# Performance work log

Hardware: AMD Instinct MI355X
Metric: run time of the kernel (lower is better)

## Reference

```python
import jax, jax.numpy as jnp
import numpy as np

B, D, H = 8192, 1024, 1024


def _linear_init(key, shape, fan_in):
    bound = 1.0 / np.sqrt(fan_in)
    return jax.random.uniform(key, shape, jnp.float32, -bound, bound)


def setup_inputs() -> dict:
    key = jax.random.key(0)
    ks = jax.random.split(key, 20)
    inp = {
        "x": jax.random.normal(ks[0], (B, D), jnp.float32),
        "h_prev": jax.random.normal(ks[1], (B, H), jnp.float32),
        "c_prev": jax.random.normal(ks[2], (B, H), jnp.float32),
        "C_prev": jax.random.normal(ks[3], (B, H), jnp.float32),
        "n_prev": jax.random.uniform(ks[4], (B, H), jnp.float32),
        "m_prev": jax.random.normal(ks[5], (B, H), jnp.float32),
    }
    # input projections Wz/Wi/Wf/Wo: Linear(D -> H) with bias
    for i, g in enumerate("ziofo"[:4]):
        pass
    names = ["z", "i", "f", "o"]
    for j, g in enumerate(names):
        inp[f"W{g}"] = _linear_init(ks[6 + j], (H, D), D)
        inp[f"b{g}"] = _linear_init(ks[10 + j], (H,), D)
        inp[f"R{g}"] = _linear_init(ks[14 + j], (H, H), H)  # no bias
    return inp


def reference(x, h_prev, c_prev, C_prev, n_prev, m_prev,
              Wz, bz, Wi, bi, Wf, bf, Wo, bo,
              Rz, Ri, Rf, Ro):
    # Batch the 4 input projections and 4 recurrent projections into 2 GEMMs.
    Wcat = jnp.concatenate([Wi, Wf, Wo, Wz], axis=0)        # [4H, D]
    bcat = jnp.concatenate([bi, bf, bo, bz], axis=0)        # [4H]
    Rcat = jnp.concatenate([Ri, Rf, Ro, Rz], axis=0)        # [4H, H]
    pre = x @ Wcat.T + bcat + h_prev @ Rcat.T               # [B, 4H]
    pi, pf, po, pz = jnp.split(pre, 4, axis=1)

    i = jnp.exp(pi)
    f = jax.nn.sigmoid(pf)
    o = jax.nn.sigmoid(po)
    z = jnp.tanh(pz)

    c = f * c_prev + i * z
    n = f * n_prev + i
    m = jnp.maximum(jnp.log(f) + m_prev, pi)  # log(exp(pi)) == pi
    h = o * (c / n)
    return (h, c, C_prev, n, m)
```

## Files before the change

kernel.cpp:

```cpp
#include <hip/hip_runtime.h>


#define B_SZ 8192
#define D_SZ 1024
#define H_SZ 1024
#define K_SZ 2048
#define N4H  4096

typedef __attribute__((ext_vector_type(4))) float f32x4;
typedef _Float16 f16;
typedef __attribute__((ext_vector_type(8))) f16 f16x8;
typedef unsigned short u16;
typedef __attribute__((ext_vector_type(4))) unsigned short u16x4;

static __device__ __forceinline__ u16 f2h(float f) {
    f16 h = (f16)f;
    return __builtin_bit_cast(unsigned short, h);
}

static __device__ __forceinline__ void load_lds16(const void* g, void* l) {
    __builtin_amdgcn_global_load_lds(
        (const __attribute__((address_space(1))) void*)g,
        (__attribute__((address_space(3))) void*)l, 16, 0, 0);
}

__global__ void convert_A(const float* __restrict__ x, const float* __restrict__ h,
                          u16* __restrict__ A) {
    const size_t nvec = (size_t)B_SZ * K_SZ / 4;
    const size_t stride = (size_t)gridDim.x * blockDim.x;
    for (size_t v = (size_t)blockIdx.x * blockDim.x + threadIdx.x; v < nvec; v += stride) {
        size_t e = v * 4;
        size_t row = e >> 11;
        int col = (int)(e & 2047);
        const float* src = (col < D_SZ) ? (x + row * D_SZ + col)
                                        : (h + row * H_SZ + (col - D_SZ));
        f32x4 val = *(const f32x4*)src;
        u16x4 o;
        o[0] = f2h(val[0]); o[1] = f2h(val[1]); o[2] = f2h(val[2]); o[3] = f2h(val[3]);
        *(u16x4*)(A + e) = o;
    }
}

__global__ void convert_W(const float* __restrict__ Wi, const float* __restrict__ Wf,
                          const float* __restrict__ Wo, const float* __restrict__ Wz,
                          const float* __restrict__ Ri, const float* __restrict__ Rf,
                          const float* __restrict__ Ro, const float* __restrict__ Rz,
                          u16* __restrict__ Wb) {
    const size_t nvec = (size_t)N4H * K_SZ / 4;
    const size_t stride = (size_t)gridDim.x * blockDim.x;
    for (size_t v = (size_t)blockIdx.x * blockDim.x + threadIdx.x; v < nvec; v += stride) {
        size_t e = v * 4;
        size_t n = e >> 11;
        int col = (int)(e & 2047);
        int g = (int)(n >> 10);
        int j = (int)(n & 1023);
        const float* Wg = (g == 0) ? Wi : (g == 1) ? Wf : (g == 2) ? Wo : Wz;
        const float* Rg = (g == 0) ? Ri : (g == 1) ? Rf : (g == 2) ? Ro : Rz;
        const float* src = (col < D_SZ) ? (Wg + (size_t)j * D_SZ + col)
                                        : (Rg + (size_t)j * H_SZ + (col - D_SZ));
        f32x4 val = *(const f32x4*)src;
        u16x4 o;
        o[0] = f2h(val[0]); o[1] = f2h(val[1]); o[2] = f2h(val[2]); o[3] = f2h(val[3]);
        *(u16x4*)(Wb + e) = o;
    }
}

__global__ __launch_bounds__(256, 2)
void gemm_pre(const u16* __restrict__ A, const u16* __restrict__ W,
              float* __restrict__ pre) {
    __shared__ u16 lA[128 * 64];
    __shared__ u16 lB[128 * 64];

    const int tid = threadIdx.x;
    const int w  = tid >> 6;
    const int l  = tid & 63;
    const int wm = w >> 1;
    const int wn = w & 1;
    const int m0 = blockIdx.x * 128;
    const int n0 = blockIdx.y * 128;

    const int lrow8 = l >> 3;
    const int lseg  = (l & 7) ^ lrow8;

    const int fr = l & 15;
    const int kq = l >> 4;

    f32x4 acc[4][4] = {};

    for (int kt = 0; kt < K_SZ; kt += 64) {
#pragma unroll
        for (int r = 0; r < 4; ++r) {
            int rowA = r * 32 + w * 8 + lrow8;
            const u16* gA = A + (size_t)(m0 + rowA) * K_SZ + kt + lseg * 8;
            load_lds16(gA, (char*)lA + (r * 32 + w * 8) * 128);
            const u16* gB = W + (size_t)(n0 + rowA) * K_SZ + kt + lseg * 8;
            load_lds16(gB, (char*)lB + (r * 32 + w * 8) * 128);
        }
        __syncthreads();

#pragma unroll
        for (int ks = 0; ks < 2; ++ks) {
            f16x8 af[4], bfr[4];
#pragma unroll
            for (int mi = 0; mi < 4; ++mi) {
                int row = wm * 64 + mi * 16 + fr;
                int seg = (ks * 4 + kq) ^ (row & 7);
                af[mi] = *(const f16x8*)&lA[row * 64 + seg * 8];
            }
#pragma unroll
            for (int ni = 0; ni < 4; ++ni) {
                int row = wn * 64 + ni * 16 + fr;
                int seg = (ks * 4 + kq) ^ (row & 7);
                bfr[ni] = *(const f16x8*)&lB[row * 64 + seg * 8];
            }
#pragma unroll
            for (int mi = 0; mi < 4; ++mi)
#pragma unroll
                for (int ni = 0; ni < 4; ++ni)
                    acc[mi][ni] = __builtin_amdgcn_mfma_f32_16x16x32_f16(
                        af[mi], bfr[ni], acc[mi][ni], 0, 0, 0);
        }
        __syncthreads();
    }

#pragma unroll
    for (int mi = 0; mi < 4; ++mi) {
#pragma unroll
        for (int ni = 0; ni < 4; ++ni) {
            int col = n0 + wn * 64 + ni * 16 + fr;
            int rbase = m0 + wm * 64 + mi * 16 + kq * 4;
#pragma unroll
            for (int r2 = 0; r2 < 4; ++r2) {
                pre[(size_t)(rbase + r2) * N4H + col] = acc[mi][ni][r2];
            }
        }
    }
}

__global__ void epilogue_k(const float* __restrict__ pre,
                           const float* __restrict__ c_prev, const float* __restrict__ C_prev,
                           const float* __restrict__ n_prev, const float* __restrict__ m_prev,
                           const float* __restrict__ bi, const float* __restrict__ bfv,
                           const float* __restrict__ bo, const float* __restrict__ bz,
                           float* __restrict__ out) {
    const size_t BH = (size_t)B_SZ * H_SZ;
    const size_t nvec = BH / 4;
    const size_t stride = (size_t)gridDim.x * blockDim.x;
    for (size_t v = (size_t)blockIdx.x * blockDim.x + threadIdx.x; v < nvec; v += stride) {
        size_t e = v * 4;
        size_t b = e >> 10;
        int j = (int)(e & 1023);
        const size_t prow = b * N4H;
        f32x4 pi4 = *(const f32x4*)&pre[prow + j]             + *(const f32x4*)&bi[j];
        f32x4 pf4 = *(const f32x4*)&pre[prow + H_SZ + j]      + *(const f32x4*)&bfv[j];
        f32x4 po4 = *(const f32x4*)&pre[prow + 2 * H_SZ + j]  + *(const f32x4*)&bo[j];
        f32x4 pz4 = *(const f32x4*)&pre[prow + 3 * H_SZ + j]  + *(const f32x4*)&bz[j];
        f32x4 cp = *(const f32x4*)&c_prev[e];
        f32x4 Cp = *(const f32x4*)&C_prev[e];
        f32x4 np = *(const f32x4*)&n_prev[e];
        f32x4 mp = *(const f32x4*)&m_prev[e];
        f32x4 ho, co, no, mo;
#pragma unroll
        for (int q = 0; q < 4; ++q) {
            float pi = pi4[q], pf = pf4[q], po = po4[q], pz = pz4[q];
            float iv = __expf(pi);
            float fv = 1.0f / (1.0f + __expf(-pf));
            float ov = 1.0f / (1.0f + __expf(-po));
            float e2 = __expf(2.0f * pz);
            float zv = 1.0f - 2.0f / (e2 + 1.0f);
            float cv = fv * cp[q] + iv * zv;
            float nv = fv * np[q] + iv;
            float mv = fmaxf(__logf(fv) + mp[q], pi);
            float hv = ov * (cv / nv);
            ho[q] = hv; co[q] = cv; no[q] = nv; mo[q] = mv;
        }
        *(f32x4*)&out[e]           = ho;
        *(f32x4*)&out[BH + e]      = co;
        *(f32x4*)&out[2 * BH + e]  = Cp;
        *(f32x4*)&out[3 * BH + e]  = no;
        *(f32x4*)&out[4 * BH + e]  = mo;
    }
}

extern "C" void kernel_launch(void* const* d_in, const int* in_sizes, int n_in,
                              void* d_out, int out_size, void* d_ws, size_t ws_size,
                              hipStream_t stream) {
    const float* x      = (const float*)d_in[0];
    const float* h_prev = (const float*)d_in[1];
    const float* c_prev = (const float*)d_in[2];
    const float* C_prev = (const float*)d_in[3];
    const float* n_prev = (const float*)d_in[4];
    const float* m_prev = (const float*)d_in[5];
    const float* Wz = (const float*)d_in[6];
    const float* bz = (const float*)d_in[7];
    const float* Rz = (const float*)d_in[8];
    const float* Wi = (const float*)d_in[9];
    const float* bi = (const float*)d_in[10];
    const float* Ri = (const float*)d_in[11];
    const float* Wf = (const float*)d_in[12];
    const float* bf = (const float*)d_in[13];
    const float* Rf = (const float*)d_in[14];
    const float* Wo = (const float*)d_in[15];
    const float* bo = (const float*)d_in[16];
    const float* Ro = (const float*)d_in[17];
    float* out = (float*)d_out;

    u16* Abuf = (u16*)d_ws;
    u16* Wbuf = (u16*)((char*)d_ws + (size_t)32 * 1024 * 1024);
    float* pre = (float*)((char*)d_ws + (size_t)48 * 1024 * 1024);

    convert_A<<<2048, 256, 0, stream>>>(x, h_prev, Abuf);
    convert_W<<<2048, 256, 0, stream>>>(Wi, Wf, Wo, Wz, Ri, Rf, Ro, Rz, Wbuf);
    gemm_pre<<<dim3(B_SZ / 128, N4H / 128), 256, 0, stream>>>(Abuf, Wbuf, pre);
    epilogue_k<<<2048, 256, 0, stream>>>(pre, c_prev, C_prev, n_prev, m_prev,
                                         bi, bf, bo, bz, out);
}
```

Measured before the change: 246.4 us.

## Fuse LSTM gate epilogue into GEMM via gate-interleaved weight layout

The weight rows are permuted during conversion so each 64-column wave tile holds 16 columns from each of the four gates. This lets the GEMM epilogue compute the gate nonlinearities and state updates directly from the accumulators. The intermediate pre-activation buffer (a large fp32 write and re-read) and the separate epilogue kernel are removed. C_prev is passed through with an async device-to-device copy. The trade-off is that the fused epilogue does scalar, strided global loads and stores instead of vectorized ones, and adds register pressure to the GEMM kernel.

```diff
diff --git a/kernel.cpp b/kernel.cpp
--- a/kernel.cpp
+++ b/kernel.cpp
@@ -50,10 +50,10 @@
     const size_t stride = (size_t)gridDim.x * blockDim.x;
     for (size_t v = (size_t)blockIdx.x * blockDim.x + threadIdx.x; v < nvec; v += stride) {
         size_t e = v * 4;
-        size_t n = e >> 11;
+        size_t r = e >> 11;
         int col = (int)(e & 2047);
-        int g = (int)(n >> 10);
-        int j = (int)(n & 1023);
+        int g = (int)(r >> 4) & 3;
+        int j = (int)((r >> 6) << 4) | (int)(r & 15);
         const float* Wg = (g == 0) ? Wi : (g == 1) ? Wf : (g == 2) ? Wo : Wz;
         const float* Rg = (g == 0) ? Ri : (g == 1) ? Rf : (g == 2) ? Ro : Rz;
         const float* src = (col < D_SZ) ? (Wg + (size_t)j * D_SZ + col)
@@ -66,8 +66,12 @@
 }
 
 __global__ __launch_bounds__(256, 2)
-void gemm_pre(const u16* __restrict__ A, const u16* __restrict__ W,
-              float* __restrict__ pre) {
+void gemm_fused(const u16* __restrict__ A, const u16* __restrict__ W,
+                const float* __restrict__ c_prev, const float* __restrict__ n_prev,
+                const float* __restrict__ m_prev,
+                const float* __restrict__ bi, const float* __restrict__ bfv,
+                const float* __restrict__ bo, const float* __restrict__ bz,
+                float* __restrict__ out) {
     __shared__ u16 lA[128 * 64];
     __shared__ u16 lB[128 * 64];
 
@@ -123,62 +127,33 @@
         __syncthreads();
     }
 
+    const size_t BH = (size_t)B_SZ * H_SZ;
+    const int j = ((n0 + wn * 64) >> 6) * 16 + fr;
+    const float bvi = bi[j], bvf = bfv[j], bvo = bo[j], bvz = bz[j];
+
 #pragma unroll
     for (int mi = 0; mi < 4; ++mi) {
+        const int rbase = m0 + wm * 64 + mi * 16 + kq * 4;
 #pragma unroll
-        for (int ni = 0; ni < 4; ++ni) {
-            int col = n0 + wn * 64 + ni * 16 + fr;
-            int rbase = m0 + wm * 64 + mi * 16 + kq * 4;
-#pragma unroll
-            for (int r2 = 0; r2 < 4; ++r2) {
-                pre[(size_t)(rbase + r2) * N4H + col] = acc[mi][ni][r2];
-            }
-        }
-    }
-}
-
-__global__ void epilogue_k(const float* __restrict__ pre,
-                           const float* __restrict__ c_prev, const float* __restrict__ C_prev,
-                           const float* __restrict__ n_prev, const float* __restrict__ m_prev,
-                           const float* __restrict__ bi, const float* __restrict__ bfv,
-                           const float* __restrict__ bo, const float* __restrict__ bz,
-                           float* __restrict__ out) {
-    const size_t BH = (size_t)B_SZ * H_SZ;
-    const size_t nvec = BH / 4;
-    const size_t stride = (size_t)gridDim.x * blockDim.x;
-    for (size_t v = (size_t)blockIdx.x * blockDim.x + threadIdx.x; v < nvec; v += stride) {
-        size_t e = v * 4;
-        size_t b = e >> 10;
-        int j = (int)(e & 1023);
-        const size_t prow = b * N4H;
-        f32x4 pi4 = *(const f32x4*)&pre[prow + j]             + *(const f32x4*)&bi[j];
-        f32x4 pf4 = *(const f32x4*)&pre[prow + H_SZ + j]      + *(const f32x4*)&bfv[j];
-        f32x4 po4 = *(const f32x4*)&pre[prow + 2 * H_SZ + j]  + *(const f32x4*)&bo[j];
-        f32x4 pz4 = *(const f32x4*)&pre[prow + 3 * H_SZ + j]  + *(const f32x4*)&bz[j];
-        f32x4 cp = *(const f32x4*)&c_prev[e];
-        f32x4 Cp = *(const f32x4*)&C_prev[e];
-        f32x4 np = *(const f32x4*)&n_prev[e];
-        f32x4 mp = *(const f32x4*)&m_prev[e];
-        f32x4 ho, co, no, mo;
-#pragma unroll
-        for (int q = 0; q < 4; ++q) {
-            float pi = pi4[q], pf = pf4[q], po = po4[q], pz = pz4[q];
+        for (int r2 = 0; r2 < 4; ++r2) {
+            const size_t idx = (size_t)(rbase + r2) * H_SZ + j;
+            float pi = acc[mi][0][r2] + bvi;
+            float pf = acc[mi][1][r2] + bvf;
+            float po = acc[mi][2][r2] + bvo;
+            float pz = acc[mi][3][r2] + bvz;
             float iv = __expf(pi);
             float fv = 1.0f / (1.0f + __expf(-pf));
             float ov = 1.0f / (1.0f + __expf(-po));
             float e2 = __expf(2.0f * pz);
             float zv = 1.0f - 2.0f / (e2 + 1.0f);
-            float cv = fv * cp[q] + iv * zv;
-            float nv = fv * np[q] + iv;
-            float mv = fmaxf(__logf(fv) + mp[q], pi);
-            float hv = ov * (cv / nv);
-            ho[q] = hv; co[q] = cv; no[q] = nv; mo[q] = mv;
+            float cv = fv * c_prev[idx] + iv * zv;
+            float nv = fv * n_prev[idx] + iv;
+            float mv = fmaxf(__logf(fv) + m_prev[idx], pi);
+            out[idx]          = ov * (cv / nv);
+            out[BH + idx]     = cv;
+            out[3 * BH + idx] = nv;
+            out[4 * BH + idx] = mv;
         }
-        *(f32x4*)&out[e]           = ho;
-        *(f32x4*)&out[BH + e]      = co;
-        *(f32x4*)&out[2 * BH + e]  = Cp;
-        *(f32x4*)&out[3 * BH + e]  = no;
-        *(f32x4*)&out[4 * BH + e]  = mo;
     }
 }
 
@@ -205,13 +180,17 @@
     const float* Ro = (const float*)d_in[17];
     float* out = (float*)d_out;
 
+    const size_t BH = (size_t)B_SZ * H_SZ;
+
     u16* Abuf = (u16*)d_ws;
     u16* Wbuf = (u16*)((char*)d_ws + (size_t)32 * 1024 * 1024);
-    float* pre = (float*)((char*)d_ws + (size_t)48 * 1024 * 1024);
 
     convert_A<<<2048, 256, 0, stream>>>(x, h_prev, Abuf);
     convert_W<<<2048, 256, 0, stream>>>(Wi, Wf, Wo, Wz, Ri, Rf, Ro, Rz, Wbuf);
-    gemm_pre<<<dim3(B_SZ / 128, N4H / 128), 256, 0, stream>>>(Abuf, Wbuf, pre);
-    epilogue_k<<<2048, 256, 0, stream>>>(pre, c_prev, C_prev, n_prev, m_prev,
-                                         bi, bf, bo, bz, out);
+
+    hipMemcpyAsync(out + 2 * BH, C_prev, BH * sizeof(float),
+                   hipMemcpyDeviceToDevice, stream);
+
+    gemm_fused<<<dim3(B_SZ / 128, N4H / 128), 256, 0, stream>>>(
+        Abuf, Wbuf, c_prev, n_prev, m_prev, bi, bf, bo, bz, out);
 }
```

New measurement: 225.8 us. 8.3% less time.
